# Optimization experiments

Hardware: AMD Instinct MI355X
Metric: run time of the kernel (lower is better)

## Reference

```python
import jax, jax.numpy as jnp
import numpy as np

KAPPA = 0.5  # decorrelation/whitening blend


def setup_inputs() -> dict:
    B, L, D, O = 8, 4096, 1024, 2048
    NS = 1024  # int(sample_frac * L) with sample_frac = 0.25
    key = jax.random.key(0)
    k1, k2, k3, k4, k5 = jax.random.split(key, 5)
    x = jax.random.normal(k1, (B, L, D), dtype=jnp.float32)
    weight = jax.random.normal(k2, (O, D), dtype=jnp.float32) * 0.02
    bias = jax.random.normal(k3, (O,), dtype=jnp.float32) * 0.02
    # decorr matrix initialized at identity; add a small perturbation so the
    # covariance/whitening statistics are non-trivial
    decorr = jnp.eye(D, dtype=jnp.float32) + 0.01 * jax.random.normal(k4, (D, D), dtype=jnp.float32)
    sample_idx = jax.random.randint(k5, (B, NS), 0, L, dtype=jnp.int64)
    return {"x": x, "weight": weight, "bias": bias, "decorr": decorr,
            "sample_idx": sample_idx}


def reference(x, weight, bias, decorr, sample_idx):
    B, L, D = x.shape
    # fused main path: y = x @ (W @ Q)^T + b
    fused = weight @ decorr                      # (O, D)
    y = jnp.einsum('bld,od->blo', x, fused) + bias

    # --- decorrelation statistics (torch.no_grad in original) ---
    sel = jnp.take_along_axis(x, sample_idx[..., None], axis=1)   # (B, NS, D)
    sd = jnp.einsum('bnd,ed->bne', sel, decorr)                   # (B, NS, D)
    sd = sd.reshape(-1, D)                                        # (N, D)
    N = sd.shape[0]

    s2 = sd * sd                                                  # (N, D)
    norm2 = jnp.sum(s2, axis=-1)                                  # (N,) = sum_i x_i^2
    s4 = jnp.sum(s2 * s2, axis=-1)                                # (N,) = sum_i x_i^4
    inv_dd = 1.0 / (D * D)
    # C = x x^T with zeroed diagonal; mean(C^2) per sample = ((sum x^2)^2 - sum x^4)/D^2
    correlation_loss = jnp.mean(norm2 * norm2 - s4) * inv_dd
    # V = diag(x^2) - I (diagonal only); mean(V^2) per sample = sum (x_i^2-1)^2 / D^2
    whitening_loss = jnp.mean(jnp.sum((s2 - 1.0) ** 2, axis=-1)) * inv_dd

    # grad = mean_b[(1-k)*C + k*V], computed from a single GEMM X^T X
    M = (sd.T @ sd) / N                                           # (D, D) mean of xx^T
    dg = jnp.mean(s2, axis=0)                                     # (D,) mean of x^2
    Dg = jnp.diag(dg)
    I = jnp.eye(D, dtype=x.dtype)
    grad = (1.0 - KAPPA) * (M - Dg) + KAPPA * (Dg - I)

    return y, grad, correlation_loss, whitening_loss
```

## Files before the change

kernel.cpp:

```cpp
#include <hip/hip_runtime.h>
#include <hip/hip_bf16.h>
#include <cstdint>

typedef unsigned short ushortT;
typedef __attribute__((ext_vector_type(8))) short short8;
typedef __attribute__((ext_vector_type(4))) float f32x4;
typedef __attribute__((ext_vector_type(4))) unsigned short us4;

__device__ __forceinline__ ushortT f2bf(float f) {
  union { float f; unsigned u; } v; v.f = f;
  unsigned r = (v.u + 0x7FFFu + ((v.u >> 16) & 1u)) >> 16;
  return (ushortT)r;
}

__device__ __forceinline__ void gl_lds16(const void* g, void* l) {
  __builtin_amdgcn_global_load_lds(
      (__attribute__((address_space(1))) void*)g,
      (__attribute__((address_space(3))) void*)l, 16, 0, 0);
}

__global__ __launch_bounds__(512, 4) void gemm256(
    const ushortT* __restrict__ A, const ushortT* __restrict__ B,
    int M, int N, int K,
    float* __restrict__ outF, const float* __restrict__ bias)
{
  __shared__ ushortT smem[3 * 256 * 32 + 3 * 128 * 32];
  ushortT(*sA)[256 * 32] = (ushortT(*)[256 * 32])smem;
  ushortT(*sB)[128 * 32] = (ushortT(*)[128 * 32])(smem + 3 * 256 * 32);

  const int tid = threadIdx.x;
  const int wv = tid >> 6, l = tid & 63;
  const int wm = wv >> 1, wn = wv & 1;

  const int bid = blockIdx.x;
  const int xcd = bid & 7, i = bid >> 3;
  const int n0 = (i & 15) * 128;
  const int m0 = (xcd * 16 + (i >> 4)) * 256;
  const int NK = K >> 5;

  f32x4 acc[4][4] = {};

  const ushortT* Ab = A + (size_t)m0 * (size_t)K;
  const ushortT* Bb = B + (size_t)n0 * (size_t)K;

  const int sr = tid >> 2;
  const int sg = tid & 3;
  const int gsw = sg ^ ((sr >> 1) & 3);

  auto stage = [&](int kt) {
    const int b = kt % 3;
    const size_t kof = (size_t)((kt << 5) + (gsw << 3));
    gl_lds16(Ab + (size_t)sr * (size_t)K + kof,         &sA[b][(wv * 16) * 32]);
    gl_lds16(Ab + (size_t)(128 + sr) * (size_t)K + kof, &sA[b][(128 + wv * 16) * 32]);
    gl_lds16(Bb + (size_t)sr * (size_t)K + kof,         &sB[b][(wv * 16) * 32]);
  };

  const int fr = l & 15;
  const int colsw = (((l >> 4) ^ ((fr >> 1) & 3)) << 3);

  stage(0);
  stage(1);

  for (int kt = 0; kt < NK; ++kt) {
    if (kt + 1 < NK) asm volatile("s_waitcnt vmcnt(3)" ::: "memory");
    else             asm volatile("s_waitcnt vmcnt(0)" ::: "memory");
    __builtin_amdgcn_s_barrier();
    if (kt + 2 < NK) stage(kt + 2);

    const int bc = kt % 3;
    short8 av[4], bv8[4];
#pragma unroll
    for (int fi = 0; fi < 4; ++fi)
      av[fi] = *(const short8*)&sA[bc][(wm * 64 + fi * 16 + fr) * 32 + colsw];
#pragma unroll
    for (int fj = 0; fj < 4; ++fj)
      bv8[fj] = *(const short8*)&sB[bc][(wn * 64 + fj * 16 + fr) * 32 + colsw];

    __builtin_amdgcn_s_setprio(1);
#pragma unroll
    for (int fi = 0; fi < 4; ++fi)
#pragma unroll
      for (int fj = 0; fj < 4; ++fj)
        acc[fi][fj] = __builtin_amdgcn_mfma_f32_16x16x32_bf16(
            av[fi], bv8[fj], acc[fi][fj], 0, 0, 0);
    __builtin_amdgcn_s_setprio(0);
  }

  const int cc = l & 15, r4 = (l >> 4) * 4;
  float bvv[4];
#pragma unroll
  for (int fj = 0; fj < 4; ++fj) bvv[fj] = bias[n0 + wn * 64 + fj * 16 + cc];

  float* lbuf = (float*)smem;
#pragma unroll
  for (int s = 0; s < 2; ++s) {
    __syncthreads();
    if ((wm >> 1) == s) {
#pragma unroll
      for (int fi = 0; fi < 4; ++fi)
#pragma unroll
        for (int r = 0; r < 4; ++r) {
          const int row = (wm & 1) * 64 + fi * 16 + r4 + r;
#pragma unroll
          for (int fj = 0; fj < 4; ++fj)
            lbuf[row * 132 + wn * 64 + fj * 16 + cc] = acc[fi][fj][r] + bvv[fj];
        }
    }
    __syncthreads();
#pragma unroll
    for (int k = 0; k < 8; ++k) {
      const int f = k * 512 + tid;
      const int row = f >> 5, c4 = f & 31;
      f32x4 v = *(const f32x4*)&lbuf[row * 132 + c4 * 4];
      __builtin_nontemporal_store(
          v, (f32x4*)&outF[(size_t)(m0 + s * 128 + row) * (size_t)N + n0 + c4 * 4]);
    }
  }
}

__global__ __launch_bounds__(256) void fused_sd(
    const ushortT* __restrict__ wbf, const ushortT* __restrict__ qT,
    ushortT* __restrict__ fusedbf,
    const ushortT* __restrict__ selbf, const ushortT* __restrict__ pbf,
    const float* __restrict__ addend,
    float* __restrict__ S2, float* __restrict__ S4,
    ushortT* __restrict__ sdT)
{
  __shared__ ushortT sA[2][128 * 32];
  __shared__ ushortT sB[2][128 * 32];
  __shared__ ushortT tbuf[128 * 136];
  const int tid = threadIdx.x;
  const int w = tid >> 6, l = tid & 63;
  const int wr = w >> 1, wc = w & 1;
  constexpr int K = 1024, NK = 32, N = 1024;

  const int bid = blockIdx.x;
  const bool isF = bid < 128;
  const int q = isF ? bid : bid - 128;
  const int m0 = isF ? (q & 15) * 128 : (q & 63) * 128;
  const int n0 = isF ? (q >> 4) * 128 : (q >> 6) * 128;
  const ushortT* A = isF ? wbf : selbf;
  const ushortT* B = isF ? qT : pbf;

  f32x4 acc[4][4] = {};

  auto stage = [&](int buf, int kt) {
    const int k0 = kt << 5;
    const size_t colA = (size_t)(k0 + (l & 3) * 8);
    const int rb = w * 16 + (l >> 2);
#pragma unroll
    for (int c = 0; c < 2; ++c) {
      gl_lds16(A + (size_t)(m0 + c * 64 + rb) * (size_t)K + colA,
               &sA[buf][c * 2048 + w * 512]);
      gl_lds16(B + (size_t)(n0 + c * 64 + rb) * (size_t)K + colA,
               &sB[buf][c * 2048 + w * 512]);
    }
  };

  stage(0, 0);
  __syncthreads();

  for (int kt = 0; kt < NK; ++kt) {
    const int buf = kt & 1;
    if (kt + 1 < NK) stage(buf ^ 1, kt + 1);
    const int ro = (l & 15) * 32 + (l >> 4) * 8;
    short8 a[4], b[4];
#pragma unroll
    for (int f = 0; f < 4; ++f) {
      a[f] = *(const short8*)&sA[buf][(wr * 64 + f * 16) * 32 + ro];
      b[f] = *(const short8*)&sB[buf][(wc * 64 + f * 16) * 32 + ro];
    }
#pragma unroll
    for (int fi = 0; fi < 4; ++fi)
#pragma unroll
      for (int fj = 0; fj < 4; ++fj)
        acc[fi][fj] = __builtin_amdgcn_mfma_f32_16x16x32_bf16(
            a[fi], b[fj], acc[fi][fj], 0, 0, 0);
    __syncthreads();
  }

  const int r4 = (l >> 4) * 4, cc = l & 15;

  if (isF) {
#pragma unroll
    for (int fi = 0; fi < 4; ++fi)
#pragma unroll
      for (int r = 0; r < 4; ++r) {
        const size_t gm = (size_t)(m0 + wr * 64 + fi * 16 + r4 + r);
#pragma unroll
        for (int fj = 0; fj < 4; ++fj) {
          const int gn = n0 + wc * 64 + fj * 16 + cc;
          fusedbf[gm * (size_t)N + gn] = f2bf(acc[fi][fj][r]);
        }
      }
  } else {
#pragma unroll
    for (int fi = 0; fi < 4; ++fi)
#pragma unroll
      for (int r = 0; r < 4; ++r) {
        const int row = wr * 64 + fi * 16 + r4 + r;
        const size_t gm = (size_t)(m0 + row);
        float rs2 = 0.f, rs4 = 0.f;
#pragma unroll
        for (int fj = 0; fj < 4; ++fj) {
          const int col = wc * 64 + fj * 16 + cc;
          float sd = acc[fi][fj][r] + addend[gm * (size_t)N + n0 + col];
          tbuf[col * 136 + row] = f2bf(sd);
          float s2 = sd * sd;
          rs2 += s2;
          rs4 += s2 * s2;
        }
#pragma unroll
        for (int mk = 1; mk < 16; mk <<= 1) {
          rs2 += __shfl_xor(rs2, mk, 16);
          rs4 += __shfl_xor(rs4, mk, 16);
        }
        if (cc == 0) { atomicAdd(&S2[gm], rs2); atomicAdd(&S4[gm], rs4); }
      }
    __syncthreads();
#pragma unroll
    for (int i = 0; i < 8; ++i) {
      const int er = i * 16 + (tid >> 4);
      const int nc = (tid & 15) * 8;
      short8 v = *(const short8*)&tbuf[er * 136 + nc];
      *(short8*)&sdT[(size_t)(n0 + er) * 8192 + m0 + nc] = v;
    }
  }
}

__global__ __launch_bounds__(256) void mgemm128sk(
    const ushortT* __restrict__ T, int Dm, int K,
    float* __restrict__ pbuf)
{
  __shared__ ushortT sA[2][128 * 32];
  __shared__ ushortT sB[2][128 * 32];
  const int tid = threadIdx.x, w = tid >> 6, l = tid & 63;
  const int wr = w >> 1, wc = w & 1;
  const int i0 = blockIdx.x * 128, j0 = blockIdx.y * 128;
  const int kt0 = blockIdx.z * 64;
  f32x4 acc[4][4] = {};

  auto stage = [&](int buf, int kt) {
    const int k0 = kt << 5;
    const size_t col = (size_t)(k0 + (l & 3) * 8);
    const int rb = w * 16 + (l >> 2);
#pragma unroll
    for (int c = 0; c < 2; ++c) {
      gl_lds16(T + (size_t)(i0 + c * 64 + rb) * (size_t)K + col,
               &sA[buf][c * 2048 + w * 512]);
      gl_lds16(T + (size_t)(j0 + c * 64 + rb) * (size_t)K + col,
               &sB[buf][c * 2048 + w * 512]);
    }
  };

  stage(0, kt0);
  __syncthreads();

  for (int t = 0; t < 64; ++t) {
    const int buf = t & 1;
    if (t + 1 < 64) stage(buf ^ 1, kt0 + t + 1);
    const int ro = (l & 15) * 32 + (l >> 4) * 8;
    short8 a[4], b[4];
#pragma unroll
    for (int f = 0; f < 4; ++f) {
      a[f] = *(const short8*)&sA[buf][(wr * 64 + f * 16) * 32 + ro];
      b[f] = *(const short8*)&sB[buf][(wc * 64 + f * 16) * 32 + ro];
    }
#pragma unroll
    for (int fi = 0; fi < 4; ++fi)
#pragma unroll
      for (int fj = 0; fj < 4; ++fj)
        acc[fi][fj] = __builtin_amdgcn_mfma_f32_16x16x32_bf16(
            a[fi], b[fj], acc[fi][fj], 0, 0, 0);
    __syncthreads();
  }

  const int r4 = (l >> 4) * 4, cc = l & 15;
  float* out = pbuf + ((size_t)blockIdx.z << 20);
#pragma unroll
  for (int fi = 0; fi < 4; ++fi)
#pragma unroll
    for (int r = 0; r < 4; ++r) {
      const int gi = i0 + wr * 64 + fi * 16 + r4 + r;
#pragma unroll
      for (int fj = 0; fj < 4; ++fj) {
        const int gj = j0 + wc * 64 + fj * 16 + cc;
        out[(size_t)gi * (size_t)Dm + gj] = acc[fi][fj][r];
      }
    }
}

__global__ __launch_bounds__(256) void finalize(
    const float* __restrict__ pbuf, float* __restrict__ grad, float invN,
    const float* __restrict__ S2, const float* __restrict__ S4,
    float* __restrict__ losses)
{
  __shared__ double red0[256];
  __shared__ double red1[256];
  const int t = threadIdx.x;
  if (blockIdx.x < 1024) {
    const int i = blockIdx.x * 256 + t;
    const size_t base = (size_t)i * 4;
    f32x4 s = *(const f32x4*)(pbuf + base) + *(const f32x4*)(pbuf + base + (1u << 20)) +
              *(const f32x4*)(pbuf + base + (2u << 20)) + *(const f32x4*)(pbuf + base + (3u << 20));
    const int row = (int)(base >> 10), c0 = (int)(base & 1023);
    f32x4 o;
#pragma unroll
    for (int j = 0; j < 4; ++j)
      o[j] = 0.5f * (s[j] * invN) - ((row == c0 + j) ? 0.5f : 0.0f);
    *(f32x4*)(grad + base) = o;
  } else {
    double ca = 0.0, wa = 0.0;
    for (int i = t; i < 8192; i += 256) {
      double s2 = (double)S2[i], s4 = (double)S4[i];
      ca += s2 * s2 - s4;
      wa += s4 - 2.0 * s2 + 1024.0;
    }
    red0[t] = ca; red1[t] = wa;
    __syncthreads();
    for (int s = 128; s > 0; s >>= 1) {
      if (t < s) { red0[t] += red0[t + s]; red1[t] += red1[t + s]; }
      __syncthreads();
    }
    if (t == 0) {
      const double inv = 1.0 / (8192.0 * 1024.0 * 1024.0);
      losses[0] = (float)(red0[0] * inv);
      losses[1] = (float)(red1[0] * inv);
    }
  }
}

__global__ __launch_bounds__(256) void prep_all(
    const float* __restrict__ x, const float* __restrict__ weight,
    const float* __restrict__ decorr, const int* __restrict__ idx,
    ushortT* __restrict__ xbf, ushortT* __restrict__ wbf,
    ushortT* __restrict__ qT, ushortT* __restrict__ pbf,
    float* __restrict__ S2S4,
    float* __restrict__ self32, ushortT* __restrict__ selbf)
{
  __shared__ float t[64][65];
  const int bid = blockIdx.x;
  const int tix = threadIdx.x;
  if (bid < 2048) {
    const f32x4* in4 = (const f32x4*)x;
    for (size_t i = (size_t)bid * 256 + tix; i < 8388608ULL; i += 2048ULL * 256) {
      f32x4 v = __builtin_nontemporal_load(&in4[i]);
      us4 o = { f2bf(v[0]), f2bf(v[1]), f2bf(v[2]), f2bf(v[3]) };
      *(us4*)(xbf + i * 4) = o;
    }
  } else if (bid < 2560) {
    const f32x4* in4 = (const f32x4*)weight;
    for (size_t i = (size_t)(bid - 2048) * 256 + tix; i < 524288ULL; i += 512ULL * 256) {
      f32x4 v = in4[i];
      us4 o = { f2bf(v[0]), f2bf(v[1]), f2bf(v[2]), f2bf(v[3]) };
      *(us4*)(wbf + i * 4) = o;
    }
  } else if (bid < 3072) {
    const size_t base = ((size_t)(bid - 2560) * 256 + tix) * 8;
    const int e = (int)(base >> 10);
    const int d0 = (int)(base & 1023);
    short8 v;
#pragma unroll
    for (int j = 0; j < 8; ++j) {
      float f = decorr[base + j] - ((e == d0 + j) ? 1.0f : 0.0f);
      v[j] = (short)f2bf(f);
    }
    *(short8*)(pbf + base) = v;
  } else if (bid < 3328) {
    const int tq = bid - 3072;
    const int bi = tq & 15, bj = tq >> 4;
    const int tr = tix >> 4, tc = tix & 15;
#pragma unroll
    for (int i = 0; i < 4; ++i) {
      const int row = i * 16 + tr;
      f32x4 v = *(const f32x4*)&decorr[(size_t)(bi * 64 + row) * 1024 + bj * 64 + tc * 4];
#pragma unroll
      for (int j = 0; j < 4; ++j) t[row][tc * 4 + j] = v[j];
    }
    __syncthreads();
#pragma unroll
    for (int i = 0; i < 4; ++i) {
      const int dr = i * 16 + tr;
      us4 o = { f2bf(t[tc * 4 + 0][dr]), f2bf(t[tc * 4 + 1][dr]),
                f2bf(t[tc * 4 + 2][dr]), f2bf(t[tc * 4 + 3][dr]) };
      *(us4*)&qT[(size_t)(bj * 64 + dr) * 1024 + bi * 64 + tc * 4] = o;
    }
  } else if (bid < 3392) {
    S2S4[(bid - 3328) * 256 + tix] = 0.f;
  } else {
    const int g = bid - 3392;
    const int b = g >> 10;
    const int row = idx[g] & 4095;
    const f32x4* src = (const f32x4*)(x + ((size_t)b * 4096 + (size_t)row) * 1024);
    f32x4 v = src[tix];
    *(f32x4*)(self32 + (size_t)g * 1024 + tix * 4) = v;
    us4 o = { f2bf(v[0]), f2bf(v[1]), f2bf(v[2]), f2bf(v[3]) };
    *(us4*)(selbf + (size_t)g * 1024 + tix * 4) = o;
  }
}

extern "C" void kernel_launch(void* const* d_in, const int* in_sizes, int n_in,
                              void* d_out, int out_size, void* d_ws, size_t ws_size,
                              hipStream_t stream) {
  (void)in_sizes; (void)n_in; (void)out_size;
  const float* x = (const float*)d_in[0];
  const float* weight = (const float*)d_in[1];
  const float* bias = (const float*)d_in[2];
  const float* decorr = (const float*)d_in[3];
  const int* sidx = (const int*)d_in[4];

  if (ws_size < 146866176ULL) return;

  char* ws = (char*)d_ws;
  ushortT* xbf     = (ushortT*)(ws);
  ushortT* fusedbf = (ushortT*)(ws + 67108864);
  ushortT* wbf     = (ushortT*)(ws + 71303168);
  ushortT* qT      = (ushortT*)(ws + 75497472);
  ushortT* pbf     = (ushortT*)(ws + 77594624);
  float*   self32  = (float*)  (ws + 79691776);
  ushortT* selbf   = (ushortT*)(ws + 113246208);
  ushortT* sdT     = (ushortT*)(ws + 130023424);
  float*   S2      = (float*)  (ws + 146800640);
  float*   S4      = (float*)  (ws + 146833408);

  float* y = (float*)d_out;
  float* grad = y + 67108864ULL;
  float* losses = grad + 1048576ULL;

  prep_all<<<dim3(11584), dim3(256), 0, stream>>>(
      x, weight, decorr, sidx, xbf, wbf, qT, pbf, S2, self32, selbf);

  fused_sd<<<dim3(640), dim3(256), 0, stream>>>(
      wbf, qT, fusedbf, selbf, pbf, self32, S2, S4, sdT);

  gemm256<<<dim3(2048), dim3(512), 0, stream>>>(
      xbf, fusedbf, 32768, 2048, 1024, y, bias);

  mgemm128sk<<<dim3(8, 8, 4), dim3(256), 0, stream>>>(sdT, 1024, 8192, self32);

  finalize<<<dim3(1025), dim3(256), 0, stream>>>(
      self32, grad, 1.0f / 8192.0f, S2, S4, losses);
}
```

Baseline: 309.1 us.

## Overlap x bf16 conversion with fused_sd and merge covariance GEMM into main GEMM

The bf16 conversion of x moves out of prep_all and into extra blocks of fused_sd, so it runs concurrently with the small fused-weight and sample-projection GEMMs. The split-K covariance GEMM is merged into the main y GEMM as 128 trailing blocks, each running two 256-thread sub-GEMMs, which removes one launch and fills the tail of the big GEMM. The launch-bounds occupancy hint drops from 4 to 2, and the merged kernel's register and LDS footprint may lower occupancy for the main GEMM path.

Measured after the change: 288.9 us. 6.5% less time.

```diff
diff --git a/kernel.cpp b/kernel.cpp
--- a/kernel.cpp
+++ b/kernel.cpp
@@ -19,102 +19,172 @@
       (__attribute__((address_space(3))) void*)l, 16, 0, 0);
 }
 
-__global__ __launch_bounds__(512, 4) void gemm256(
+__global__ __launch_bounds__(512, 2) void gemm_mg(
     const ushortT* __restrict__ A, const ushortT* __restrict__ B,
-    int M, int N, int K,
-    float* __restrict__ outF, const float* __restrict__ bias)
+    float* __restrict__ outF, const float* __restrict__ bias,
+    const ushortT* __restrict__ T, float* __restrict__ pbuf)
 {
-  __shared__ ushortT smem[3 * 256 * 32 + 3 * 128 * 32];
-  ushortT(*sA)[256 * 32] = (ushortT(*)[256 * 32])smem;
-  ushortT(*sB)[128 * 32] = (ushortT(*)[128 * 32])(smem + 3 * 256 * 32);
-
+  __shared__ ushortT smem[36864];
   const int tid = threadIdx.x;
-  const int wv = tid >> 6, l = tid & 63;
-  const int wm = wv >> 1, wn = wv & 1;
-
   const int bid = blockIdx.x;
-  const int xcd = bid & 7, i = bid >> 3;
-  const int n0 = (i & 15) * 128;
-  const int m0 = (xcd * 16 + (i >> 4)) * 256;
-  const int NK = K >> 5;
-
-  f32x4 acc[4][4] = {};
-
-  const ushortT* Ab = A + (size_t)m0 * (size_t)K;
-  const ushortT* Bb = B + (size_t)n0 * (size_t)K;
-
-  const int sr = tid >> 2;
-  const int sg = tid & 3;
-  const int gsw = sg ^ ((sr >> 1) & 3);
-
-  auto stage = [&](int kt) {
-    const int b = kt % 3;
-    const size_t kof = (size_t)((kt << 5) + (gsw << 3));
-    gl_lds16(Ab + (size_t)sr * (size_t)K + kof,         &sA[b][(wv * 16) * 32]);
-    gl_lds16(Ab + (size_t)(128 + sr) * (size_t)K + kof, &sA[b][(128 + wv * 16) * 32]);
-    gl_lds16(Bb + (size_t)sr * (size_t)K + kof,         &sB[b][(wv * 16) * 32]);
-  };
-
-  const int fr = l & 15;
-  const int colsw = (((l >> 4) ^ ((fr >> 1) & 3)) << 3);
-
-  stage(0);
-  stage(1);
-
-  for (int kt = 0; kt < NK; ++kt) {
-    if (kt + 1 < NK) asm volatile("s_waitcnt vmcnt(3)" ::: "memory");
-    else             asm volatile("s_waitcnt vmcnt(0)" ::: "memory");
-    __builtin_amdgcn_s_barrier();
-    if (kt + 2 < NK) stage(kt + 2);
-
-    const int bc = kt % 3;
-    short8 av[4], bv8[4];
+  constexpr int M = 32768, N = 2048, K = 1024;
+
+  if (bid < 2048) {
+    ushortT(*sA)[256 * 32] = (ushortT(*)[256 * 32])smem;
+    ushortT(*sB)[128 * 32] = (ushortT(*)[128 * 32])(smem + 3 * 256 * 32);
+
+    const int wv = tid >> 6, l = tid & 63;
+    const int wm = wv >> 1, wn = wv & 1;
+
+    const int xcd = bid & 7, i = bid >> 3;
+    const int n0 = (i & 15) * 128;
+    const int m0 = (xcd * 16 + (i >> 4)) * 256;
+    const int NK = K >> 5;
+
+    f32x4 acc[4][4] = {};
+
+    const ushortT* Ab = A + (size_t)m0 * (size_t)K;
+    const ushortT* Bb = B + (size_t)n0 * (size_t)K;
+
+    const int sr = tid >> 2;
+    const int sg = tid & 3;
+    const int gsw = sg ^ ((sr >> 1) & 3);
+
+    auto stage = [&](int kt) {
+      const int b = kt % 3;
+      const size_t kof = (size_t)((kt << 5) + (gsw << 3));
+      gl_lds16(Ab + (size_t)sr * (size_t)K + kof,         &sA[b][(wv * 16) * 32]);
+      gl_lds16(Ab + (size_t)(128 + sr) * (size_t)K + kof, &sA[b][(128 + wv * 16) * 32]);
+      gl_lds16(Bb + (size_t)sr * (size_t)K + kof,         &sB[b][(wv * 16) * 32]);
+    };
+
+    const int fr = l & 15;
+    const int colsw = (((l >> 4) ^ ((fr >> 1) & 3)) << 3);
+
+    stage(0);
+    stage(1);
+
+    for (int kt = 0; kt < NK; ++kt) {
+      if (kt + 1 < NK) asm volatile("s_waitcnt vmcnt(3)" ::: "memory");
+      else             asm volatile("s_waitcnt vmcnt(0)" ::: "memory");
+      __builtin_amdgcn_s_barrier();
+      if (kt + 2 < NK) stage(kt + 2);
+
+      const int bc = kt % 3;
+      short8 av[4], bv8[4];
+#pragma unroll
+      for (int fi = 0; fi < 4; ++fi)
+        av[fi] = *(const short8*)&sA[bc][(wm * 64 + fi * 16 + fr) * 32 + colsw];
+#pragma unroll
+      for (int fj = 0; fj < 4; ++fj)
+        bv8[fj] = *(const short8*)&sB[bc][(wn * 64 + fj * 16 + fr) * 32 + colsw];
+
+      __builtin_amdgcn_s_setprio(1);
+#pragma unroll
+      for (int fi = 0; fi < 4; ++fi)
+#pragma unroll
+        for (int fj = 0; fj < 4; ++fj)
+          acc[fi][fj] = __builtin_amdgcn_mfma_f32_16x16x32_bf16(
+              av[fi], bv8[fj], acc[fi][fj], 0, 0, 0);
+      __builtin_amdgcn_s_setprio(0);
+    }
+
+    const int cc = l & 15, r4 = (l >> 4) * 4;
+    float bvv[4];
+#pragma unroll
+    for (int fj = 0; fj < 4; ++fj) bvv[fj] = bias[n0 + wn * 64 + fj * 16 + cc];
+
+    float* lbuf = (float*)smem;
+#pragma unroll
+    for (int s = 0; s < 2; ++s) {
+      __syncthreads();
+      if ((wm >> 1) == s) {
+#pragma unroll
+        for (int fi = 0; fi < 4; ++fi)
+#pragma unroll
+          for (int r = 0; r < 4; ++r) {
+            const int row = (wm & 1) * 64 + fi * 16 + r4 + r;
+#pragma unroll
+            for (int fj = 0; fj < 4; ++fj)
+              lbuf[row * 132 + wn * 64 + fj * 16 + cc] = acc[fi][fj][r] + bvv[fj];
+          }
+      }
+      __syncthreads();
+#pragma unroll
+      for (int k = 0; k < 8; ++k) {
+        const int f = k * 512 + tid;
+        const int row = f >> 5, c4 = f & 31;
+        f32x4 v = *(const f32x4*)&lbuf[row * 132 + c4 * 4];
+        __builtin_nontemporal_store(
+            v, (f32x4*)&outF[(size_t)(m0 + s * 128 + row) * (size_t)N + n0 + c4 * 4]);
+      }
+    }
+  } else {
+    const int tt = bid - 2048;
+    const int g = tid >> 8;
+    const int lt = tid & 255;
+    const int q = tt * 2 + g;
+    const int i0 = (q & 7) * 128;
+    const int j0 = ((q >> 3) & 7) * 128;
+    const int kt0 = (q >> 6) * 64;
+    constexpr int Kt = 8192, Dm = 1024;
+
+    ushortT* pool = smem + g * 16384;
+    ushortT(*sA)[128 * 32] = (ushortT(*)[128 * 32])pool;
+    ushortT(*sB)[128 * 32] = (ushortT(*)[128 * 32])(pool + 2 * 128 * 32);
+
+    const int w = lt >> 6, l = lt & 63;
+    const int wr = w >> 1, wc = w & 1;
+    f32x4 acc[4][4] = {};
+
+    auto stage = [&](int buf, int kt) {
+      const int k0 = kt << 5;
+      const size_t col = (size_t)(k0 + (l & 3) * 8);
+      const int rb = w * 16 + (l >> 2);
+#pragma unroll
+      for (int c = 0; c < 2; ++c) {
+        gl_lds16(T + (size_t)(i0 + c * 64 + rb) * (size_t)Kt + col,
+                 &sA[buf][c * 2048 + w * 512]);
+        gl_lds16(T + (size_t)(j0 + c * 64 + rb) * (size_t)Kt + col,
+                 &sB[buf][c * 2048 + w * 512]);
+      }
+    };
+
+    stage(0, kt0);
+    __syncthreads();
+
+    for (int t = 0; t < 64; ++t) {
+      const int buf = t & 1;
+      if (t + 1 < 64) stage(buf ^ 1, kt0 + t + 1);
+      const int ro = (l & 15) * 32 + (l >> 4) * 8;
+      short8 a[4], b[4];
+#pragma unroll
+      for (int f = 0; f < 4; ++f) {
+        a[f] = *(const short8*)&sA[buf][(wr * 64 + f * 16) * 32 + ro];
+        b[f] = *(const short8*)&sB[buf][(wc * 64 + f * 16) * 32 + ro];
+      }
+#pragma unroll
+      for (int fi = 0; fi < 4; ++fi)
+#pragma unroll
+        for (int fj = 0; fj < 4; ++fj)
+          acc[fi][fj] = __builtin_amdgcn_mfma_f32_16x16x32_bf16(
+              a[fi], b[fj], acc[fi][fj], 0, 0, 0);
+      __syncthreads();
+    }
+
+    const int r4 = (l >> 4) * 4, cc = l & 15;
+    float* out = pbuf + ((size_t)(q >> 6) << 20);
 #pragma unroll
     for (int fi = 0; fi < 4; ++fi)
-      av[fi] = *(const short8*)&sA[bc][(wm * 64 + fi * 16 + fr) * 32 + colsw];
-#pragma unroll
-    for (int fj = 0; fj < 4; ++fj)
-      bv8[fj] = *(const short8*)&sB[bc][(wn * 64 + fj * 16 + fr) * 32 + colsw];
-
-    __builtin_amdgcn_s_setprio(1);
-#pragma unroll
-    for (int fi = 0; fi < 4; ++fi)
-#pragma unroll
-      for (int fj = 0; fj < 4; ++fj)
-        acc[fi][fj] = __builtin_amdgcn_mfma_f32_16x16x32_bf16(
-            av[fi], bv8[fj], acc[fi][fj], 0, 0, 0);
-    __builtin_amdgcn_s_setprio(0);
-  }
-
-  const int cc = l & 15, r4 = (l >> 4) * 4;
-  float bvv[4];
-#pragma unroll
-  for (int fj = 0; fj < 4; ++fj) bvv[fj] = bias[n0 + wn * 64 + fj * 16 + cc];
-
-  float* lbuf = (float*)smem;
-#pragma unroll
-  for (int s = 0; s < 2; ++s) {
-    __syncthreads();
-    if ((wm >> 1) == s) {
-#pragma unroll
-      for (int fi = 0; fi < 4; ++fi)
-#pragma unroll
-        for (int r = 0; r < 4; ++r) {
-          const int row = (wm & 1) * 64 + fi * 16 + r4 + r;
-#pragma unroll
-          for (int fj = 0; fj < 4; ++fj)
-            lbuf[row * 132 + wn * 64 + fj * 16 + cc] = acc[fi][fj][r] + bvv[fj];
+#pragma unroll
+      for (int r = 0; r < 4; ++r) {
+        const int gi = i0 + wr * 64 + fi * 16 + r4 + r;
+#pragma unroll
+        for (int fj = 0; fj < 4; ++fj) {
+          const int gj = j0 + wc * 64 + fj * 16 + cc;
+          out[(size_t)gi * (size_t)Dm + gj] = acc[fi][fj][r];
         }
-    }
-    __syncthreads();
-#pragma unroll
-    for (int k = 0; k < 8; ++k) {
-      const int f = k * 512 + tid;
-      const int row = f >> 5, c4 = f & 31;
-      f32x4 v = *(const f32x4*)&lbuf[row * 132 + c4 * 4];
-      __builtin_nontemporal_store(
-          v, (f32x4*)&outF[(size_t)(m0 + s * 128 + row) * (size_t)N + n0 + c4 * 4]);
-    }
+      }
   }
 }
 
@@ -124,17 +194,32 @@
     const ushortT* __restrict__ selbf, const ushortT* __restrict__ pbf,
     const float* __restrict__ addend,
     float* __restrict__ S2, float* __restrict__ S4,
-    ushortT* __restrict__ sdT)
+    ushortT* __restrict__ sdT,
+    const float* __restrict__ x, ushortT* __restrict__ xbf)
 {
-  __shared__ ushortT sA[2][128 * 32];
-  __shared__ ushortT sB[2][128 * 32];
-  __shared__ ushortT tbuf[128 * 136];
+  __shared__ ushortT smem[17408];
   const int tid = threadIdx.x;
+  const int bid = blockIdx.x;
+
+  if (bid >= 640) {
+    const f32x4* in4 = (const f32x4*)x;
+    for (size_t i = (size_t)(bid - 640) * 256 + tid; i < 8388608ULL;
+         i += 2048ULL * 256) {
+      f32x4 v = __builtin_nontemporal_load(&in4[i]);
+      us4 o = { f2bf(v[0]), f2bf(v[1]), f2bf(v[2]), f2bf(v[3]) };
+      *(us4*)(xbf + i * 4) = o;
+    }
+    return;
+  }
+
+  ushortT(*sA)[128 * 32] = (ushortT(*)[128 * 32])smem;
+  ushortT(*sB)[128 * 32] = (ushortT(*)[128 * 32])(smem + 2 * 128 * 32);
+  ushortT* tbuf = smem;
+
   const int w = tid >> 6, l = tid & 63;
   const int wr = w >> 1, wc = w & 1;
   constexpr int K = 1024, NK = 32, N = 1024;
 
-  const int bid = blockIdx.x;
   const bool isF = bid < 128;
   const int q = isF ? bid : bid - 128;
   const int m0 = isF ? (q & 15) * 128 : (q & 63) * 128;
@@ -226,68 +311,6 @@
       *(short8*)&sdT[(size_t)(n0 + er) * 8192 + m0 + nc] = v;
     }
   }
-}
-
-__global__ __launch_bounds__(256) void mgemm128sk(
-    const ushortT* __restrict__ T, int Dm, int K,
-    float* __restrict__ pbuf)
-{
-  __shared__ ushortT sA[2][128 * 32];
-  __shared__ ushortT sB[2][128 * 32];
-  const int tid = threadIdx.x, w = tid >> 6, l = tid & 63;
-  const int wr = w >> 1, wc = w & 1;
-  const int i0 = blockIdx.x * 128, j0 = blockIdx.y * 128;
-  const int kt0 = blockIdx.z * 64;
-  f32x4 acc[4][4] = {};
-
-  auto stage = [&](int buf, int kt) {
-    const int k0 = kt << 5;
-    const size_t col = (size_t)(k0 + (l & 3) * 8);
-    const int rb = w * 16 + (l >> 2);
-#pragma unroll
-    for (int c = 0; c < 2; ++c) {
-      gl_lds16(T + (size_t)(i0 + c * 64 + rb) * (size_t)K + col,
-               &sA[buf][c * 2048 + w * 512]);
-      gl_lds16(T + (size_t)(j0 + c * 64 + rb) * (size_t)K + col,
-               &sB[buf][c * 2048 + w * 512]);
-    }
-  };
-
-  stage(0, kt0);
-  __syncthreads();
-
-  for (int t = 0; t < 64; ++t) {
-    const int buf = t & 1;
-    if (t + 1 < 64) stage(buf ^ 1, kt0 + t + 1);
-    const int ro = (l & 15) * 32 + (l >> 4) * 8;
-    short8 a[4], b[4];
-#pragma unroll
-    for (int f = 0; f < 4; ++f) {
-      a[f] = *(const short8*)&sA[buf][(wr * 64 + f * 16) * 32 + ro];
-      b[f] = *(const short8*)&sB[buf][(wc * 64 + f * 16) * 32 + ro];
-    }
-#pragma unroll
-    for (int fi = 0; fi < 4; ++fi)
-#pragma unroll
-      for (int fj = 0; fj < 4; ++fj)
-        acc[fi][fj] = __builtin_amdgcn_mfma_f32_16x16x32_bf16(
-            a[fi], b[fj], acc[fi][fj], 0, 0, 0);
-    __syncthreads();
-  }
-
-  const int r4 = (l >> 4) * 4, cc = l & 15;
-  float* out = pbuf + ((size_t)blockIdx.z << 20);
-#pragma unroll
-  for (int fi = 0; fi < 4; ++fi)
-#pragma unroll
-    for (int r = 0; r < 4; ++r) {
-      const int gi = i0 + wr * 64 + fi * 16 + r4 + r;
-#pragma unroll
-      for (int fj = 0; fj < 4; ++fj) {
-        const int gj = j0 + wc * 64 + fj * 16 + cc;
-        out[(size_t)gi * (size_t)Dm + gj] = acc[fi][fj][r];
-      }
-    }
 }
 
 __global__ __launch_bounds__(256) void finalize(
@@ -333,30 +356,22 @@
 __global__ __launch_bounds__(256) void prep_all(
     const float* __restrict__ x, const float* __restrict__ weight,
     const float* __restrict__ decorr, const int* __restrict__ idx,
-    ushortT* __restrict__ xbf, ushortT* __restrict__ wbf,
-    ushortT* __restrict__ qT, ushortT* __restrict__ pbf,
-    float* __restrict__ S2S4,
+    ushortT* __restrict__ wbf, ushortT* __restrict__ qT,
+    ushortT* __restrict__ pbf, float* __restrict__ S2S4,
     float* __restrict__ self32, ushortT* __restrict__ selbf)
 {
   __shared__ float t[64][65];
   const int bid = blockIdx.x;
   const int tix = threadIdx.x;
-  if (bid < 2048) {
-    const f32x4* in4 = (const f32x4*)x;
-    for (size_t i = (size_t)bid * 256 + tix; i < 8388608ULL; i += 2048ULL * 256) {
-      f32x4 v = __builtin_nontemporal_load(&in4[i]);
-      us4 o = { f2bf(v[0]), f2bf(v[1]), f2bf(v[2]), f2bf(v[3]) };
-      *(us4*)(xbf + i * 4) = o;
-    }
-  } else if (bid < 2560) {
+  if (bid < 512) {
     const f32x4* in4 = (const f32x4*)weight;
-    for (size_t i = (size_t)(bid - 2048) * 256 + tix; i < 524288ULL; i += 512ULL * 256) {
+    for (size_t i = (size_t)bid * 256 + tix; i < 524288ULL; i += 512ULL * 256) {
       f32x4 v = in4[i];
       us4 o = { f2bf(v[0]), f2bf(v[1]), f2bf(v[2]), f2bf(v[3]) };
       *(us4*)(wbf + i * 4) = o;
     }
-  } else if (bid < 3072) {
-    const size_t base = ((size_t)(bid - 2560) * 256 + tix) * 8;
+  } else if (bid < 1024) {
+    const size_t base = ((size_t)(bid - 512) * 256 + tix) * 8;
     const int e = (int)(base >> 10);
     const int d0 = (int)(base & 1023);
     short8 v;
@@ -366,8 +381,8 @@
       v[j] = (short)f2bf(f);
     }
     *(short8*)(pbf + base) = v;
-  } else if (bid < 3328) {
-    const int tq = bid - 3072;
+  } else if (bid < 1280) {
+    const int tq = bid - 1024;
     const int bi = tq & 15, bj = tq >> 4;
     const int tr = tix >> 4, tc = tix & 15;
 #pragma unroll
@@ -385,10 +400,10 @@
                 f2bf(t[tc * 4 + 2][dr]), f2bf(t[tc * 4 + 3][dr]) };
       *(us4*)&qT[(size_t)(bj * 64 + dr) * 1024 + bi * 64 + tc * 4] = o;
     }
-  } else if (bid < 3392) {
-    S2S4[(bid - 3328) * 256 + tix] = 0.f;
+  } else if (bid < 1344) {
+    S2S4[(bid - 1280) * 256 + tix] = 0.f;
   } else {
-    const int g = bid - 3392;
+    const int g = bid - 1344;
     const int b = g >> 10;
     const int row = idx[g] & 4095;
     const f32x4* src = (const f32x4*)(x + ((size_t)b * 4096 + (size_t)row) * 1024);
@@ -427,16 +442,14 @@
   float* grad = y + 67108864ULL;
   float* losses = grad + 1048576ULL;
 
-  prep_all<<<dim3(11584), dim3(256), 0, stream>>>(
-      x, weight, decorr, sidx, xbf, wbf, qT, pbf, S2, self32, selbf);
-
-  fused_sd<<<dim3(640), dim3(256), 0, stream>>>(
-      wbf, qT, fusedbf, selbf, pbf, self32, S2, S4, sdT);
-
-  gemm256<<<dim3(2048), dim3(512), 0, stream>>>(
-      xbf, fusedbf, 32768, 2048, 1024, y, bias);
-
-  mgemm128sk<<<dim3(8, 8, 4), dim3(256), 0, stream>>>(sdT, 1024, 8192, self32);
+  prep_all<<<dim3(9536), dim3(256), 0, stream>>>(
+      x, weight, decorr, sidx, wbf, qT, pbf, S2, self32, selbf);
+
+  fused_sd<<<dim3(2688), dim3(256), 0, stream>>>(
+      wbf, qT, fusedbf, selbf, pbf, self32, S2, S4, sdT, x, xbf);
+
+  gemm_mg<<<dim3(2176), dim3(512), 0, stream>>>(
+      xbf, fusedbf, y, bias, sdT, self32);
 
   finalize<<<dim3(1025), dim3(256), 0, stream>>>(
       self32, grad, 1.0f / 8192.0f, S2, S4, losses);
```
